# Kernel tuning notes

Hardware: AMD Instinct MI355X
Metric: run time of the kernel (lower is better)

The kernel has to match this reference:

```python
import jax, jax.numpy as jnp
import numpy as np

B, C, H, W = 4, 128, 64, 64


def setup_inputs() -> dict:
    key = jax.random.key(0)
    ks = jax.random.split(key, 7)
    s = 1.0 / np.sqrt(C)  # torch Conv2d default init scale (uniform bound)
    x = jax.random.normal(ks[0], (B, C, H, W), dtype=jnp.float32)
    Wq = jax.random.uniform(ks[1], (C, C), jnp.float32, -s, s)
    bq = jax.random.uniform(ks[2], (C,), jnp.float32, -s, s)
    Wk = jax.random.uniform(ks[3], (C, C), jnp.float32, -s, s)
    bk = jax.random.uniform(ks[4], (C,), jnp.float32, -s, s)
    Wv = jax.random.uniform(ks[5], (C, C), jnp.float32, -s, s)
    bv = jax.random.uniform(ks[6], (C,), jnp.float32, -s, s)
    return {"x": x, "Wq": Wq, "bq": bq, "Wk": Wk, "bk": bk, "Wv": Wv, "bv": bv}


def _conv1x1_flat(x_flat, Wt, b):
    # x_flat: [B, C, N]; 1x1 conv == channel matmul
    return jnp.einsum('oc,bcn->bon', Wt, x_flat) + b[None, :, None]


def reference(x, Wq, bq, Wk, bk, Wv, bv):
    b_, c_, h_, w_ = x.shape
    n = h_ * w_
    xf = x.reshape(b_, c_, n)
    k_map = _conv1x1_flat(xf, Wk, bk)              # [B, C, N]
    q_map = _conv1x1_flat(xf, Wq, bq)              # [B, C, N]
    v_map = _conv1x1_flat(xf, Wv, bv)              # [B, C, N]
    energy = jnp.einsum('bci,bcj->bij', q_map, k_map)   # [B, N, N]
    attention = jax.nn.softmax(energy, axis=-1)
    # out[b,c,i] = sum_j v[b,c,j] * attention[b,i,j]  (v @ attention^T)
    out = jnp.einsum('bcj,bij->bci', v_map, attention)  # [B, C, N]
    return x + out.reshape(b_, c_, h_, w_)
```

## Files before the change

kernel.cpp:

```cpp
#include <hip/hip_runtime.h>

#define B_ 4
#define C_ 128
#define N_ 4096
#define LOG2E 1.44269504088896340736f
#define KB_PER_B (C_ * N_ * 2)

typedef __bf16 bf16x8 __attribute__((ext_vector_type(8)));
typedef __bf16 bf16x4 __attribute__((ext_vector_type(4)));
typedef float  f32x16 __attribute__((ext_vector_type(16)));
typedef int    i32x4  __attribute__((ext_vector_type(4)));

static __device__ __forceinline__ void stage16(const void* g_lane, char* lds_base, int lane16) {
#if __has_builtin(__builtin_amdgcn_global_load_lds)
    __builtin_amdgcn_global_load_lds(
        (const __attribute__((address_space(1))) void*)g_lane,
        (__attribute__((address_space(3))) void*)lds_base, 16, 0, 0);
    (void)lane16;
#else
    *(i32x4*)(lds_base + lane16) = *(const i32x4*)g_lane;
#endif
}

__global__ __launch_bounds__(256) void proj_kernel(
    const float* __restrict__ x,
    const float* __restrict__ Wq, const float* __restrict__ bq,
    const float* __restrict__ Wk, const float* __restrict__ bk,
    const float* __restrict__ Wv, const float* __restrict__ bv,
    unsigned short* __restrict__ qT, char* __restrict__ kQ,
    char* __restrict__ vQ)
{
    __shared__ __align__(16) char wlds[32768];

    const int tid  = threadIdx.x;
    const int wave = tid >> 6;
    const int lane = tid & 63;
    const int col  = lane & 31;
    const int h    = lane >> 5;

    const int jw  = blockIdx.x * 4 + wave;
    const int mat = jw >> 9;
    const int rem = jw & 511;
    const int b   = rem >> 7;
    const int nb  = rem & 127;
    const int n   = nb * 32 + col;

    const float* W    = (mat == 0) ? Wq : (mat == 1) ? Wk : Wv;
    const float* bias = (mat == 0) ? bq : (mat == 1) ? bk : bv;
    const float  scale = (mat == 0) ? LOG2E : 1.0f;

    #pragma unroll
    for (int k = 0; k < 16; ++k) {
        const int q = tid + k * 256;
        const int o = q >> 5;
        const int g = q & 31;
        float4 w = *((const float4*)W + q);
        bf16x4 d;
        d[0] = (__bf16)(w.x * scale); d[1] = (__bf16)(w.y * scale);
        d[2] = (__bf16)(w.z * scale); d[3] = (__bf16)(w.w * scale);
        *(bf16x4*)(wlds + o * 256 + ((((g >> 1) ^ (o & 15)) << 4) | ((g & 1) * 8))) = d;
    }
    __syncthreads();

    bf16x8 xf[8];
    const float* xcol = x + (size_t)b * C_ * N_ + n;
    #pragma unroll
    for (int ch = 0; ch < 8; ++ch) {
        const int c0 = ch * 16 + 8 * h;
        bf16x8 v;
        #pragma unroll
        for (int e = 0; e < 8; ++e) v[e] = (__bf16)xcol[(size_t)(c0 + e) * N_];
        xf[ch] = v;
    }

    f32x16 acc[4];
    #pragma unroll
    for (int ob = 0; ob < 4; ++ob)
        #pragma unroll
        for (int rr = 0; rr < 16; ++rr) acc[ob][rr] = 0.0f;

    #pragma unroll
    for (int ch = 0; ch < 8; ++ch) {
        #pragma unroll
        for (int ob = 0; ob < 4; ++ob) {
            const char* wrow = wlds + (ob * 32 + col) * 256;
            bf16x8 wf = __builtin_bit_cast(bf16x8,
                *(const i32x4*)(wrow + (((ch * 2 + h) ^ (col & 15)) << 4)));
            acc[ob] = __builtin_amdgcn_mfma_f32_32x32x16_bf16(
                wf, xf[ch], acc[ob], 0, 0, 0);
        }
    }

    if (mat == 0) {
        unsigned short* dst = qT + (size_t)(b * N_ + n) * C_;
        #pragma unroll
        for (int ob = 0; ob < 4; ++ob) {
            #pragma unroll
            for (int qd = 0; qd < 4; ++qd) {
                const int obase = ob * 32 + 8 * qd + 4 * h;
                bf16x4 d;
                d[0] = (__bf16)(acc[ob][4 * qd + 0] + bias[obase + 0] * scale);
                d[1] = (__bf16)(acc[ob][4 * qd + 1] + bias[obase + 1] * scale);
                d[2] = (__bf16)(acc[ob][4 * qd + 2] + bias[obase + 2] * scale);
                d[3] = (__bf16)(acc[ob][4 * qd + 3] + bias[obase + 3] * scale);
                *(bf16x4*)(dst + obase) = d;
            }
        }
    } else if (mat == 1) {
        const int kt = (nb & 1) * 32 + col;
        char* dst = kQ + (size_t)b * KB_PER_B + (size_t)(nb >> 1) * 16384 + kt * 256;
        const int kx = kt & 15;
        #pragma unroll
        for (int ob = 0; ob < 4; ++ob) {
            #pragma unroll
            for (int qd = 0; qd < 4; ++qd) {
                const int obase = ob * 32 + 8 * qd + 4 * h;
                bf16x4 d;
                d[0] = (__bf16)(acc[ob][4 * qd + 0] + bias[obase + 0]);
                d[1] = (__bf16)(acc[ob][4 * qd + 1] + bias[obase + 1]);
                d[2] = (__bf16)(acc[ob][4 * qd + 2] + bias[obase + 2]);
                d[3] = (__bf16)(acc[ob][4 * qd + 3] + bias[obase + 3]);
                *(bf16x4*)(dst + ((((ob * 4 + qd) ^ kx) << 4) | (8 * h))) = d;
            }
        }
    } else {
        char* dst = vQ + (size_t)b * KB_PER_B + (size_t)(nb >> 1) * 16384;
        const int kt  = (nb & 1) * 32 + col;
        const int m   = kt >> 4;
        const int w16 = kt & 15;
        const int hk  = (w16 >> 2) & 1;
        const int pos = (w16 & 3) | (((w16 >> 3) & 1) << 2);
        #pragma unroll
        for (int ob = 0; ob < 4; ++ob) {
            #pragma unroll
            for (int rr = 0; rr < 16; ++rr) {
                const int o = ob * 32 + (rr & 3) + 8 * (rr >> 2) + 4 * h;
                const int R = o >> 1;
                const int cidx = (o & 1) * 8 + 2 * m + hk;
                *(unsigned short*)(dst + R * 256 + (((cidx ^ (R & 15)) << 4)) + pos * 2) =
                    __builtin_bit_cast(unsigned short,
                                       (__bf16)(acc[ob][rr] + bias[o]));
            }
        }
    }
}

template<int NS>
__global__ __launch_bounds__(256, 2) void attn_kernel(
    const unsigned short* __restrict__ qT,
    const char* __restrict__ kQ,
    const char* __restrict__ vQ,
    unsigned short* __restrict__ pO,
    float* __restrict__ lG)
{
    __shared__ __align__(16) char smem[65536];

    const int tid  = threadIdx.x;
    const int w    = tid >> 6;
    const int lane = tid & 63;
    const int l31  = lane & 31;
    const int h    = lane >> 5;

    const int orig = blockIdx.x;
    const int b    = (orig & 7) >> 1;
    const int idx  = ((orig >> 3) << 1) | (orig & 1);
    const int part = idx % NS;
    const int qg   = idx / NS;
    const int i0   = qg * 128 + w * 32;

    const int NT = N_ / (NS * 64);
    const char* kq0 = kQ + (size_t)b * KB_PER_B + (size_t)(part * NT) * 16384;
    const char* vq0 = vQ + (size_t)b * KB_PER_B + (size_t)(part * NT) * 16384;

    bf16x8 qf[8];
    {
        const unsigned short* qrow = qT + (size_t)(b * N_ + i0 + l31) * C_;
        #pragma unroll
        for (int ch = 0; ch < 8; ++ch)
            qf[ch] = __builtin_bit_cast(bf16x8, *(const i32x4*)(qrow + ch * 16 + 8 * h));
    }
    bf16x8 ones;
    #pragma unroll
    for (int e = 0; e < 8; ++e) ones[e] = (__bf16)1.0f;

    f32x16 accO[4];
    #pragma unroll
    for (int cb = 0; cb < 4; ++cb)
        #pragma unroll
        for (int rr = 0; rr < 16; ++rr) accO[cb][rr] = 0.0f;
    f32x16 ls;
    #pragma unroll
    for (int rr = 0; rr < 16; ++rr) ls[rr] = 0.0f;

    const int lane16 = lane * 16;
    auto stage = [&](int t, char* buf) {
        const char* g = ((w < 2) ? kq0 : vq0) + (size_t)t * 16384 + (w & 1) * 8192 + lane16;
        char* d = buf + (w >> 1) * 16384 + (w & 1) * 8192;
        #pragma unroll
        for (int u = 0; u < 8; ++u)
            stage16(g + u * 1024, d + u * 1024, lane16);
    };

    stage(0, smem);
    __syncthreads();
    int cur = 0;

    #pragma unroll 1
    for (int t = 0; t < NT; ++t) {
        char* kb = smem + cur * 32768;
        char* vb = kb + 16384;
        if (t + 1 < NT) stage(t + 1, smem + (cur ^ 1) * 32768);

        f32x16 e0, e1;
        #pragma unroll
        for (int rr = 0; rr < 16; ++rr) { e0[rr] = 0.0f; e1[rr] = 0.0f; }
        {
            const char* kr0 = kb + l31 * 256;
            const int   kx  = l31 & 15;
            __builtin_amdgcn_s_setprio(1);
            #pragma unroll
            for (int ch = 0; ch < 8; ++ch) {
                const int off = ((2 * ch + h) ^ kx) << 4;
                bf16x8 k0 = __builtin_bit_cast(bf16x8, *(const i32x4*)(kr0 + off));
                e0 = __builtin_amdgcn_mfma_f32_32x32x16_bf16(k0, qf[ch], e0, 0, 0, 0);
                bf16x8 k1 = __builtin_bit_cast(bf16x8, *(const i32x4*)(kr0 + 8192 + off));
                e1 = __builtin_amdgcn_mfma_f32_32x32x16_bf16(k1, qf[ch], e1, 0, 0, 0);
            }
            __builtin_amdgcn_s_setprio(0);
        }

        #pragma unroll
        for (int rr = 0; rr < 16; ++rr) {
            e0[rr] = exp2f(e0[rr]);
            e1[rr] = exp2f(e1[rr]);
        }

        bf16x8 pf[4];
        #pragma unroll
        for (int m = 0; m < 4; ++m) {
            bf16x8 p;
            #pragma unroll
            for (int e = 0; e < 8; ++e)
                p[e] = (__bf16)((m < 2) ? e0[(m & 1) * 8 + e] : e1[(m & 1) * 8 + e]);
            pf[m] = p;
        }

        __builtin_amdgcn_s_setprio(1);
        #pragma unroll
        for (int m = 0; m < 4; ++m)
            ls = __builtin_amdgcn_mfma_f32_32x32x16_bf16(ones, pf[m], ls, 0, 0, 0);
        {
            const int rsw = l31 >> 1;
            const int ci  = (l31 & 1) * 8;
            #pragma unroll
            for (int cb = 0; cb < 4; ++cb) {
                const char* vrow = vb + (cb * 16 + (l31 >> 1)) * 256;
                #pragma unroll
                for (int m = 0; m < 4; ++m) {
                    bf16x8 vf = __builtin_bit_cast(bf16x8,
                        *(const i32x4*)(vrow + (((ci + 2 * m + h) ^ rsw) << 4)));
                    accO[cb] = __builtin_amdgcn_mfma_f32_32x32x16_bf16(
                        vf, pf[m], accO[cb], 0, 0, 0);
                }
            }
        }
        __builtin_amdgcn_s_setprio(0);

        __syncthreads();
        cur ^= 1;
    }

    if (h == 0)
        lG[((size_t)part * B_ + b) * N_ + i0 + l31] = ls[0];

    unsigned short* pOq = pO + ((size_t)part * B_ + b) * C_ * N_;
    #pragma unroll
    for (int cb = 0; cb < 4; ++cb) {
        #pragma unroll
        for (int rr = 0; rr < 16; ++rr) {
            const int c = cb * 32 + (rr & 3) + 8 * (rr >> 2) + 4 * h;
            pOq[(size_t)c * N_ + i0 + l31] =
                __builtin_bit_cast(unsigned short, (__bf16)accO[cb][rr]);
        }
    }
}

template<int NS>
__global__ __launch_bounds__(256) void merge_kernel(
    const float* __restrict__ x,
    const unsigned short* __restrict__ pO,
    const float* __restrict__ lG,
    float* __restrict__ out)
{
    const int idx = blockIdx.x * 256 + threadIdx.x;
    const int nq  = idx & (N_ / 4 - 1);
    const int bc  = idx >> 10;
    const int b   = bc >> 7;
    const size_t off = (size_t)bc * N_ + nq * 4;

    float4 xv = *(const float4*)(x + off);

    float num[4] = {0, 0, 0, 0}, den[4] = {0, 0, 0, 0};
    #pragma unroll
    for (int q = 0; q < NS; ++q) {
        bf16x4 r = *(const bf16x4*)(pO + (size_t)q * B_ * C_ * N_ + off);
        const float* lp = lG + ((size_t)q * B_ + b) * N_ + nq * 4;
        #pragma unroll
        for (int j = 0; j < 4; ++j) {
            num[j] += (float)r[j];
            den[j] += lp[j];
        }
    }
    float4 ov;
    ov.x = xv.x + num[0] / den[0];
    ov.y = xv.y + num[1] / den[1];
    ov.z = xv.z + num[2] / den[2];
    ov.w = xv.w + num[3] / den[3];
    *(float4*)(out + off) = ov;
}

extern "C" void kernel_launch(void* const* d_in, const int* in_sizes, int n_in,
                              void* d_out, int out_size, void* d_ws, size_t ws_size,
                              hipStream_t stream)
{
    const float* x  = (const float*)d_in[0];
    const float* Wq = (const float*)d_in[1];
    const float* bq = (const float*)d_in[2];
    const float* Wk = (const float*)d_in[3];
    const float* bk = (const float*)d_in[4];
    const float* Wv = (const float*)d_in[5];
    const float* bv = (const float*)d_in[6];
    float* out = (float*)d_out;

    unsigned short* qT = (unsigned short*)d_ws;
    char* kQ = (char*)(qT + (size_t)B_ * N_ * C_);
    char* vQ = kQ + (size_t)B_ * KB_PER_B;
    unsigned short* pO = (unsigned short*)(vQ + (size_t)B_ * KB_PER_B);

    const size_t slotO = (size_t)B_ * C_ * N_;
    const size_t slotL = (size_t)B_ * N_;
    const size_t base  = 3ull * B_ * N_ * C_ * 2;
    const size_t need4 = base + 4 * (slotO * 2 + slotL * 4);
    const int nMerge = (B_ * C_ * N_ / 4) / 256;

    proj_kernel<<<384, 256, 0, stream>>>(x, Wq, bq, Wk, bk, Wv, bv, qT, kQ, vQ);

    if (ws_size >= need4) {
        float* lG = (float*)(pO + 4 * slotO);
        attn_kernel<4><<<B_ * (N_ / 128) * 4, 256, 0, stream>>>(qT, kQ, vQ, pO, lG);
        merge_kernel<4><<<nMerge, 256, 0, stream>>>(x, pO, lG, out);
    } else {
        float* lG = (float*)(pO + 2 * slotO);
        attn_kernel<2><<<B_ * (N_ / 128) * 2, 256, 0, stream>>>(qT, kQ, vQ, pO, lG);
        merge_kernel<2><<<nMerge, 256, 0, stream>>>(x, pO, lG, out);
    }
}
```

Before: 67.19 us.

## Single-buffer V in LDS, compute row sums in VALU, add 8-way key split

```diff
diff --git a/kernel.cpp b/kernel.cpp
--- a/kernel.cpp
+++ b/kernel.cpp
@@ -146,14 +146,14 @@
 }
 
 template<int NS>
-__global__ __launch_bounds__(256, 2) void attn_kernel(
+__global__ __launch_bounds__(256, 3) void attn_kernel(
     const unsigned short* __restrict__ qT,
     const char* __restrict__ kQ,
     const char* __restrict__ vQ,
     unsigned short* __restrict__ pO,
     float* __restrict__ lG)
 {
-    __shared__ __align__(16) char smem[65536];
+    __shared__ __align__(16) char smem[49152];
 
     const int tid  = threadIdx.x;
     const int w    = tid >> 6;
@@ -171,6 +171,7 @@
     const int NT = N_ / (NS * 64);
     const char* kq0 = kQ + (size_t)b * KB_PER_B + (size_t)(part * NT) * 16384;
     const char* vq0 = vQ + (size_t)b * KB_PER_B + (size_t)(part * NT) * 16384;
+    char* vbuf = smem + 32768;
 
     bf16x8 qf[8];
     {
@@ -179,37 +180,39 @@
         for (int ch = 0; ch < 8; ++ch)
             qf[ch] = __builtin_bit_cast(bf16x8, *(const i32x4*)(qrow + ch * 16 + 8 * h));
     }
-    bf16x8 ones;
-    #pragma unroll
-    for (int e = 0; e < 8; ++e) ones[e] = (__bf16)1.0f;
 
     f32x16 accO[4];
     #pragma unroll
     for (int cb = 0; cb < 4; ++cb)
         #pragma unroll
         for (int rr = 0; rr < 16; ++rr) accO[cb][rr] = 0.0f;
-    f32x16 ls;
-    #pragma unroll
-    for (int rr = 0; rr < 16; ++rr) ls[rr] = 0.0f;
+    float l_run = 0.0f;
 
     const int lane16 = lane * 16;
-    auto stage = [&](int t, char* buf) {
-        const char* g = ((w < 2) ? kq0 : vq0) + (size_t)t * 16384 + (w & 1) * 8192 + lane16;
-        char* d = buf + (w >> 1) * 16384 + (w & 1) * 8192;
-        #pragma unroll
-        for (int u = 0; u < 8; ++u)
+    auto stageK = [&](int t, char* kd) {
+        const char* g = kq0 + (size_t)t * 16384 + w * 4096 + lane16;
+        char* d = kd + w * 4096;
+        #pragma unroll
+        for (int u = 0; u < 4; ++u)
             stage16(g + u * 1024, d + u * 1024, lane16);
     };
-
-    stage(0, smem);
+    auto stageV = [&](int t) {
+        const char* g = vq0 + (size_t)t * 16384 + w * 4096 + lane16;
+        char* d = vbuf + w * 4096;
+        #pragma unroll
+        for (int u = 0; u < 4; ++u)
+            stage16(g + u * 1024, d + u * 1024, lane16);
+    };
+
+    stageK(0, smem);
     __syncthreads();
     int cur = 0;
 
     #pragma unroll 1
     for (int t = 0; t < NT; ++t) {
-        char* kb = smem + cur * 32768;
-        char* vb = kb + 16384;
-        if (t + 1 < NT) stage(t + 1, smem + (cur ^ 1) * 32768);
+        char* kb = smem + cur * 16384;
+        stageV(t);
+        if (t + 1 < NT) stageK(t + 1, smem + (cur ^ 1) * 16384);
 
         f32x16 e0, e1;
         #pragma unroll
@@ -235,6 +238,11 @@
             e1[rr] = exp2f(e1[rr]);
         }
 
+        float lsum = 0.0f;
+        #pragma unroll
+        for (int rr = 0; rr < 16; ++rr) lsum += e0[rr] + e1[rr];
+        l_run += lsum;
+
         bf16x8 pf[4];
         #pragma unroll
         for (int m = 0; m < 4; ++m) {
@@ -245,16 +253,15 @@
             pf[m] = p;
         }
 
-        __builtin_amdgcn_s_setprio(1);
-        #pragma unroll
-        for (int m = 0; m < 4; ++m)
-            ls = __builtin_amdgcn_mfma_f32_32x32x16_bf16(ones, pf[m], ls, 0, 0, 0);
+        __syncthreads();
+
         {
             const int rsw = l31 >> 1;
             const int ci  = (l31 & 1) * 8;
+            __builtin_amdgcn_s_setprio(1);
             #pragma unroll
             for (int cb = 0; cb < 4; ++cb) {
-                const char* vrow = vb + (cb * 16 + (l31 >> 1)) * 256;
+                const char* vrow = vbuf + (cb * 16 + (l31 >> 1)) * 256;
                 #pragma unroll
                 for (int m = 0; m < 4; ++m) {
                     bf16x8 vf = __builtin_bit_cast(bf16x8,
@@ -263,15 +270,16 @@
                         vf, pf[m], accO[cb], 0, 0, 0);
                 }
             }
-        }
-        __builtin_amdgcn_s_setprio(0);
+            __builtin_amdgcn_s_setprio(0);
+        }
 
         __syncthreads();
         cur ^= 1;
     }
 
+    l_run += __shfl_xor(l_run, 32, 64);
     if (h == 0)
-        lG[((size_t)part * B_ + b) * N_ + i0 + l31] = ls[0];
+        lG[((size_t)part * B_ + b) * N_ + i0 + l31] = l_run;
 
     unsigned short* pOq = pO + ((size_t)part * B_ + b) * C_ * N_;
     #pragma unroll
@@ -340,12 +348,17 @@
     const size_t slotO = (size_t)B_ * C_ * N_;
     const size_t slotL = (size_t)B_ * N_;
     const size_t base  = 3ull * B_ * N_ * C_ * 2;
+    const size_t need8 = base + 8 * (slotO * 2 + slotL * 4);
     const size_t need4 = base + 4 * (slotO * 2 + slotL * 4);
     const int nMerge = (B_ * C_ * N_ / 4) / 256;
 
     proj_kernel<<<384, 256, 0, stream>>>(x, Wq, bq, Wk, bk, Wv, bv, qT, kQ, vQ);
 
-    if (ws_size >= need4) {
+    if (ws_size >= need8) {
+        float* lG = (float*)(pO + 8 * slotO);
+        attn_kernel<8><<<B_ * (N_ / 128) * 8, 256, 0, stream>>>(qT, kQ, vQ, pO, lG);
+        merge_kernel<8><<<nMerge, 256, 0, stream>>>(x, pO, lG, out);
+    } else if (ws_size >= need4) {
         float* lG = (float*)(pO + 4 * slotO);
         attn_kernel<4><<<B_ * (N_ / 128) * 4, 256, 0, stream>>>(qT, kQ, vQ, pO, lG);
         merge_kernel<4><<<nMerge, 256, 0, stream>>>(x, pO, lG, out);
```

Result: slower. 70.78 us (+5.3%).

## Software-pipeline QK of next tile with softmax-exp and PV of previous tile

Applied to the files above, without the earlier changes.

```diff
diff --git a/kernel.cpp b/kernel.cpp
--- a/kernel.cpp
+++ b/kernel.cpp
@@ -171,6 +171,8 @@
     const int NT = N_ / (NS * 64);
     const char* kq0 = kQ + (size_t)b * KB_PER_B + (size_t)(part * NT) * 16384;
     const char* vq0 = vQ + (size_t)b * KB_PER_B + (size_t)(part * NT) * 16384;
+    char* kbufs = smem;
+    char* vbufs = smem + 32768;
 
     bf16x8 qf[8];
     {
@@ -193,82 +195,100 @@
     for (int rr = 0; rr < 16; ++rr) ls[rr] = 0.0f;
 
     const int lane16 = lane * 16;
-    auto stage = [&](int t, char* buf) {
-        const char* g = ((w < 2) ? kq0 : vq0) + (size_t)t * 16384 + (w & 1) * 8192 + lane16;
-        char* d = buf + (w >> 1) * 16384 + (w & 1) * 8192;
-        #pragma unroll
-        for (int u = 0; u < 8; ++u)
+    auto stageK = [&](int t, int buf) {
+        const char* g = kq0 + (size_t)t * 16384 + w * 4096 + lane16;
+        char* d = kbufs + buf * 16384 + w * 4096;
+        #pragma unroll
+        for (int u = 0; u < 4; ++u)
             stage16(g + u * 1024, d + u * 1024, lane16);
     };
-
-    stage(0, smem);
-    __syncthreads();
-    int cur = 0;
-
-    #pragma unroll 1
-    for (int t = 0; t < NT; ++t) {
-        char* kb = smem + cur * 32768;
-        char* vb = kb + 16384;
-        if (t + 1 < NT) stage(t + 1, smem + (cur ^ 1) * 32768);
-
-        f32x16 e0, e1;
-        #pragma unroll
-        for (int rr = 0; rr < 16; ++rr) { e0[rr] = 0.0f; e1[rr] = 0.0f; }
-        {
-            const char* kr0 = kb + l31 * 256;
-            const int   kx  = l31 & 15;
-            __builtin_amdgcn_s_setprio(1);
-            #pragma unroll
-            for (int ch = 0; ch < 8; ++ch) {
-                const int off = ((2 * ch + h) ^ kx) << 4;
-                bf16x8 k0 = __builtin_bit_cast(bf16x8, *(const i32x4*)(kr0 + off));
-                e0 = __builtin_amdgcn_mfma_f32_32x32x16_bf16(k0, qf[ch], e0, 0, 0, 0);
-                bf16x8 k1 = __builtin_bit_cast(bf16x8, *(const i32x4*)(kr0 + 8192 + off));
-                e1 = __builtin_amdgcn_mfma_f32_32x32x16_bf16(k1, qf[ch], e1, 0, 0, 0);
-            }
-            __builtin_amdgcn_s_setprio(0);
-        }
-
+    auto stageV = [&](int t, int buf) {
+        const char* g = vq0 + (size_t)t * 16384 + w * 4096 + lane16;
+        char* d = vbufs + buf * 16384 + w * 4096;
+        #pragma unroll
+        for (int u = 0; u < 4; ++u)
+            stage16(g + u * 1024, d + u * 1024, lane16);
+    };
+
+    const int kx = l31 & 15;
+    auto QK = [&](int buf, f32x16& o0, f32x16& o1) {
+        const char* kr0 = kbufs + buf * 16384 + l31 * 256;
+        #pragma unroll
+        for (int rr = 0; rr < 16; ++rr) { o0[rr] = 0.0f; o1[rr] = 0.0f; }
+        __builtin_amdgcn_s_setprio(1);
+        #pragma unroll
+        for (int ch = 0; ch < 8; ++ch) {
+            const int off = ((2 * ch + h) ^ kx) << 4;
+            bf16x8 k0 = __builtin_bit_cast(bf16x8, *(const i32x4*)(kr0 + off));
+            o0 = __builtin_amdgcn_mfma_f32_32x32x16_bf16(k0, qf[ch], o0, 0, 0, 0);
+            bf16x8 k1 = __builtin_bit_cast(bf16x8, *(const i32x4*)(kr0 + 8192 + off));
+            o1 = __builtin_amdgcn_mfma_f32_32x32x16_bf16(k1, qf[ch], o1, 0, 0, 0);
+        }
+        __builtin_amdgcn_s_setprio(0);
+    };
+
+    const int rsw = l31 >> 1;
+    const int ci  = (l31 & 1) * 8;
+    auto FIN = [&](int buf, const f32x16& s0, const f32x16& s1) {
+        float p0[16], p1[16];
         #pragma unroll
         for (int rr = 0; rr < 16; ++rr) {
-            e0[rr] = exp2f(e0[rr]);
-            e1[rr] = exp2f(e1[rr]);
-        }
-
+            p0[rr] = exp2f(s0[rr]);
+            p1[rr] = exp2f(s1[rr]);
+        }
         bf16x8 pf[4];
         #pragma unroll
         for (int m = 0; m < 4; ++m) {
             bf16x8 p;
             #pragma unroll
             for (int e = 0; e < 8; ++e)
-                p[e] = (__bf16)((m < 2) ? e0[(m & 1) * 8 + e] : e1[(m & 1) * 8 + e]);
+                p[e] = (__bf16)((m < 2) ? p0[(m & 1) * 8 + e] : p1[(m & 1) * 8 + e]);
             pf[m] = p;
         }
-
         __builtin_amdgcn_s_setprio(1);
         #pragma unroll
         for (int m = 0; m < 4; ++m)
             ls = __builtin_amdgcn_mfma_f32_32x32x16_bf16(ones, pf[m], ls, 0, 0, 0);
-        {
-            const int rsw = l31 >> 1;
-            const int ci  = (l31 & 1) * 8;
-            #pragma unroll
-            for (int cb = 0; cb < 4; ++cb) {
-                const char* vrow = vb + (cb * 16 + (l31 >> 1)) * 256;
-                #pragma unroll
-                for (int m = 0; m < 4; ++m) {
-                    bf16x8 vf = __builtin_bit_cast(bf16x8,
-                        *(const i32x4*)(vrow + (((ci + 2 * m + h) ^ rsw) << 4)));
-                    accO[cb] = __builtin_amdgcn_mfma_f32_32x32x16_bf16(
-                        vf, pf[m], accO[cb], 0, 0, 0);
-                }
+        const char* vbase = vbufs + buf * 16384;
+        #pragma unroll
+        for (int cb = 0; cb < 4; ++cb) {
+            const char* vrow = vbase + (cb * 16 + (l31 >> 1)) * 256;
+            #pragma unroll
+            for (int m = 0; m < 4; ++m) {
+                bf16x8 vf = __builtin_bit_cast(bf16x8,
+                    *(const i32x4*)(vrow + (((ci + 2 * m + h) ^ rsw) << 4)));
+                accO[cb] = __builtin_amdgcn_mfma_f32_32x32x16_bf16(
+                    vf, pf[m], accO[cb], 0, 0, 0);
             }
         }
         __builtin_amdgcn_s_setprio(0);
+    };
+
+    f32x16 s0, s1;
+
+    stageK(0, 0);
+    __syncthreads();
+    stageK(1, 1);
+    stageV(0, 1);
+    QK(0, s0, s1);
+    __syncthreads();
+    int cur = 1;
+
+    #pragma unroll 2
+    for (int t = 1; t < NT; ++t) {
+        if (t + 1 < NT) stageK(t + 1, cur ^ 1);
+        stageV(t, cur ^ 1);
+
+        f32x16 e0, e1;
+        QK(cur, e0, e1);
+        FIN(cur, s0, s1);
+        s0 = e0; s1 = e1;
 
         __syncthreads();
         cur ^= 1;
     }
+
+    FIN(cur, s0, s1);
 
     if (h == 0)
         lG[((size_t)part * B_ + b) * N_ + i0 + l31] = ls[0];
```

New measurement: 66.71 us. No clear change (-0.7%).

## Load K/V tiles directly into registers instead of staging through LDS

Applied to the files above, without the earlier changes.

```diff
diff --git a/kernel.cpp b/kernel.cpp
--- a/kernel.cpp
+++ b/kernel.cpp
@@ -10,17 +10,6 @@
 typedef __bf16 bf16x4 __attribute__((ext_vector_type(4)));
 typedef float  f32x16 __attribute__((ext_vector_type(16)));
 typedef int    i32x4  __attribute__((ext_vector_type(4)));
-
-static __device__ __forceinline__ void stage16(const void* g_lane, char* lds_base, int lane16) {
-#if __has_builtin(__builtin_amdgcn_global_load_lds)
-    __builtin_amdgcn_global_load_lds(
-        (const __attribute__((address_space(1))) void*)g_lane,
-        (__attribute__((address_space(3))) void*)lds_base, 16, 0, 0);
-    (void)lane16;
-#else
-    *(i32x4*)(lds_base + lane16) = *(const i32x4*)g_lane;
-#endif
-}
 
 __global__ __launch_bounds__(256) void proj_kernel(
     const float* __restrict__ x,
@@ -107,9 +96,7 @@
             }
         }
     } else if (mat == 1) {
-        const int kt = (nb & 1) * 32 + col;
-        char* dst = kQ + (size_t)b * KB_PER_B + (size_t)(nb >> 1) * 16384 + kt * 256;
-        const int kx = kt & 15;
+        char* dst = kQ + (size_t)b * KB_PER_B + (size_t)nb * 8192 + col * 16 + 8 * h;
         #pragma unroll
         for (int ob = 0; ob < 4; ++ob) {
             #pragma unroll
@@ -120,24 +107,22 @@
                 d[1] = (__bf16)(acc[ob][4 * qd + 1] + bias[obase + 1]);
                 d[2] = (__bf16)(acc[ob][4 * qd + 2] + bias[obase + 2]);
                 d[3] = (__bf16)(acc[ob][4 * qd + 3] + bias[obase + 3]);
-                *(bf16x4*)(dst + ((((ob * 4 + qd) ^ kx) << 4) | (8 * h))) = d;
+                *(bf16x4*)(dst + (ob * 4 + qd) * 512) = d;
             }
         }
     } else {
-        char* dst = vQ + (size_t)b * KB_PER_B + (size_t)(nb >> 1) * 16384;
-        const int kt  = (nb & 1) * 32 + col;
-        const int m   = kt >> 4;
-        const int w16 = kt & 15;
-        const int hk  = (w16 >> 2) & 1;
-        const int pos = (w16 & 3) | (((w16 >> 3) & 1) << 2);
+        char* dst = vQ + (size_t)b * KB_PER_B + (size_t)nb * 8192;
+        const int m  = (col >> 4) & 1;
+        const int w16 = col & 15;
+        const int hv = (w16 >> 2) & 1;
+        const int e  = (w16 & 3) | ((w16 >> 3) << 2);
         #pragma unroll
         for (int ob = 0; ob < 4; ++ob) {
             #pragma unroll
             for (int rr = 0; rr < 16; ++rr) {
                 const int o = ob * 32 + (rr & 3) + 8 * (rr >> 2) + 4 * h;
-                const int R = o >> 1;
-                const int cidx = (o & 1) * 8 + 2 * m + hk;
-                *(unsigned short*)(dst + R * 256 + (((cidx ^ (R & 15)) << 4)) + pos * 2) =
+                *(unsigned short*)(dst + (ob * 4 + m * 2 + hv) * 512
+                                       + (o & 31) * 16 + e * 2) =
                     __builtin_bit_cast(unsigned short,
                                        (__bf16)(acc[ob][rr] + bias[o]));
             }
@@ -153,8 +138,6 @@
     unsigned short* __restrict__ pO,
     float* __restrict__ lG)
 {
-    __shared__ __align__(16) char smem[65536];
-
     const int tid  = threadIdx.x;
     const int w    = tid >> 6;
     const int lane = tid & 63;
@@ -168,9 +151,10 @@
     const int qg   = idx / NS;
     const int i0   = qg * 128 + w * 32;
 
-    const int NT = N_ / (NS * 64);
-    const char* kq0 = kQ + (size_t)b * KB_PER_B + (size_t)(part * NT) * 16384;
-    const char* vq0 = vQ + (size_t)b * KB_PER_B + (size_t)(part * NT) * 16384;
+    const int NT = N_ / (NS * 32);
+    const char* kq0 = kQ + (size_t)b * KB_PER_B + (size_t)(part * NT) * 8192;
+    const char* vq0 = vQ + (size_t)b * KB_PER_B + (size_t)(part * NT) * 8192;
+    const int lbase = h * 512 + l31 * 16;
 
     bf16x8 qf[8];
     {
@@ -179,99 +163,75 @@
         for (int ch = 0; ch < 8; ++ch)
             qf[ch] = __builtin_bit_cast(bf16x8, *(const i32x4*)(qrow + ch * 16 + 8 * h));
     }
-    bf16x8 ones;
-    #pragma unroll
-    for (int e = 0; e < 8; ++e) ones[e] = (__bf16)1.0f;
 
     f32x16 accO[4];
     #pragma unroll
     for (int cb = 0; cb < 4; ++cb)
         #pragma unroll
         for (int rr = 0; rr < 16; ++rr) accO[cb][rr] = 0.0f;
-    f32x16 ls;
-    #pragma unroll
-    for (int rr = 0; rr < 16; ++rr) ls[rr] = 0.0f;
-
-    const int lane16 = lane * 16;
-    auto stage = [&](int t, char* buf) {
-        const char* g = ((w < 2) ? kq0 : vq0) + (size_t)t * 16384 + (w & 1) * 8192 + lane16;
-        char* d = buf + (w >> 1) * 16384 + (w & 1) * 8192;
+    float l_run = 0.0f;
+
+    i32x4 kreg[8], vreg[8];
+    auto loadK = [&](int t) {
+        const char* ka = kq0 + (size_t)t * 8192 + lbase;
+        #pragma unroll
+        for (int ch = 0; ch < 8; ++ch)
+            kreg[ch] = *(const i32x4*)(ka + ch * 1024);
+    };
+    auto loadV = [&](int t) {
+        const char* va = vq0 + (size_t)t * 8192 + lbase;
         #pragma unroll
         for (int u = 0; u < 8; ++u)
-            stage16(g + u * 1024, d + u * 1024, lane16);
+            vreg[u] = *(const i32x4*)(va + u * 1024);
     };
 
-    stage(0, smem);
-    __syncthreads();
-    int cur = 0;
+    loadK(0);
+    loadV(0);
 
     #pragma unroll 1
     for (int t = 0; t < NT; ++t) {
-        char* kb = smem + cur * 32768;
-        char* vb = kb + 16384;
-        if (t + 1 < NT) stage(t + 1, smem + (cur ^ 1) * 32768);
-
-        f32x16 e0, e1;
-        #pragma unroll
-        for (int rr = 0; rr < 16; ++rr) { e0[rr] = 0.0f; e1[rr] = 0.0f; }
-        {
-            const char* kr0 = kb + l31 * 256;
-            const int   kx  = l31 & 15;
-            __builtin_amdgcn_s_setprio(1);
-            #pragma unroll
-            for (int ch = 0; ch < 8; ++ch) {
-                const int off = ((2 * ch + h) ^ kx) << 4;
-                bf16x8 k0 = __builtin_bit_cast(bf16x8, *(const i32x4*)(kr0 + off));
-                e0 = __builtin_amdgcn_mfma_f32_32x32x16_bf16(k0, qf[ch], e0, 0, 0, 0);
-                bf16x8 k1 = __builtin_bit_cast(bf16x8, *(const i32x4*)(kr0 + 8192 + off));
-                e1 = __builtin_amdgcn_mfma_f32_32x32x16_bf16(k1, qf[ch], e1, 0, 0, 0);
-            }
-            __builtin_amdgcn_s_setprio(0);
-        }
-
-        #pragma unroll
-        for (int rr = 0; rr < 16; ++rr) {
-            e0[rr] = exp2f(e0[rr]);
-            e1[rr] = exp2f(e1[rr]);
-        }
-
-        bf16x8 pf[4];
-        #pragma unroll
-        for (int m = 0; m < 4; ++m) {
+        f32x16 e;
+        #pragma unroll
+        for (int rr = 0; rr < 16; ++rr) e[rr] = 0.0f;
+        __builtin_amdgcn_s_setprio(1);
+        #pragma unroll
+        for (int ch = 0; ch < 8; ++ch)
+            e = __builtin_amdgcn_mfma_f32_32x32x16_bf16(
+                __builtin_bit_cast(bf16x8, kreg[ch]), qf[ch], e, 0, 0, 0);
+        __builtin_amdgcn_s_setprio(0);
+
+        if (t + 1 < NT) loadK(t + 1);
+
+        float lsum = 0.0f;
+        #pragma unroll
+        for (int rr = 0; rr < 16; ++rr) { e[rr] = exp2f(e[rr]); lsum += e[rr]; }
+        l_run += lsum;
+
+        bf16x8 pf[2];
+        #pragma unroll
+        for (int m = 0; m < 2; ++m) {
             bf16x8 p;
             #pragma unroll
-            for (int e = 0; e < 8; ++e)
-                p[e] = (__bf16)((m < 2) ? e0[(m & 1) * 8 + e] : e1[(m & 1) * 8 + e]);
+            for (int ee = 0; ee < 8; ++ee) p[ee] = (__bf16)e[m * 8 + ee];
             pf[m] = p;
         }
 
         __builtin_amdgcn_s_setprio(1);
         #pragma unroll
-        for (int m = 0; m < 4; ++m)
-            ls = __builtin_amdgcn_mfma_f32_32x32x16_bf16(ones, pf[m], ls, 0, 0, 0);
-        {
-            const int rsw = l31 >> 1;
-            const int ci  = (l31 & 1) * 8;
-            #pragma unroll
-            for (int cb = 0; cb < 4; ++cb) {
-                const char* vrow = vb + (cb * 16 + (l31 >> 1)) * 256;
-                #pragma unroll
-                for (int m = 0; m < 4; ++m) {
-                    bf16x8 vf = __builtin_bit_cast(bf16x8,
-                        *(const i32x4*)(vrow + (((ci + 2 * m + h) ^ rsw) << 4)));
-                    accO[cb] = __builtin_amdgcn_mfma_f32_32x32x16_bf16(
-                        vf, pf[m], accO[cb], 0, 0, 0);
-                }
-            }
+        for (int cb = 0; cb < 4; ++cb) {
+            accO[cb] = __builtin_amdgcn_mfma_f32_32x32x16_bf16(
+                __builtin_bit_cast(bf16x8, vreg[cb * 2 + 0]), pf[0], accO[cb], 0, 0, 0);
+            accO[cb] = __builtin_amdgcn_mfma_f32_32x32x16_bf16(
+                __builtin_bit_cast(bf16x8, vreg[cb * 2 + 1]), pf[1], accO[cb], 0, 0, 0);
         }
         __builtin_amdgcn_s_setprio(0);
 
-        __syncthreads();
-        cur ^= 1;
-    }
-
+        if (t + 1 < NT) loadV(t + 1);
+    }
+
+    l_run += __shfl_xor(l_run, 32, 64);
     if (h == 0)
-        lG[((size_t)part * B_ + b) * N_ + i0 + l31] = ls[0];
+        lG[((size_t)part * B_ + b) * N_ + i0 + l31] = l_run;
 
     unsigned short* pOq = pO + ((size_t)part * B_ + b) * C_ * N_;
     #pragma unroll
```

After: 71.42 us (median of 2 runs). 1.06x slower.
